# Kernel optimization log

Hardware: AMD Instinct MI355X
Metric: run time of the kernel (lower is better)

The kernel has to match this reference:

```python
import jax, jax.numpy as jnp
import numpy as np

SEGMENT_LENGTHS = [2048, 4096, 8192]
DILATION_RATES = [1, 2, 4]


def setup_inputs() -> dict:
    key = jax.random.key(0)
    kq, kk, kv = jax.random.split(key, 3)
    shape = (4, 8192, 16, 64)  # [b, seq, heads, head_dim]
    return {
        "query": jax.random.normal(kq, shape, dtype=jnp.float32),
        "key": jax.random.normal(kk, shape, dtype=jnp.float32),
        "value": jax.random.normal(kv, shape, dtype=jnp.float32),
    }


def _dilated_attention(query, key, value):
    b, S, h, d = query.shape
    num_groups = len(DILATION_RATES)
    # replicate torch group-size logic: h // ng each, first (h % ng) get +1
    group_sizes = [h // num_groups] * num_groups
    for i in range(h % num_groups):
        group_sizes[i] += 1

    scale = 1.0 / jnp.sqrt(jnp.asarray(d, dtype=query.dtype))
    out = jnp.zeros_like(query)

    for i, (g, r, s) in enumerate(zip(group_sizes, DILATION_RATES, SEGMENT_LENGTHS)):
        n = S // s
        offset = i % r
        hmin, hmax = i * g, (i + 1) * g  # faithful to original (uses current g)

        # gather strided segment views: [b, n, s', g, d]
        q = query.reshape(b, n, s, h, d)[:, :, offset::r, hmin:hmax, :]
        k = key.reshape(b, n, s, h, d)[:, :, offset::r, hmin:hmax, :]
        v = value.reshape(b, n, s, h, d)[:, :, offset::r, hmin:hmax, :]

        # NOTE: the original SDPA is applied to [., s', g, d], so attention
        # runs over the HEAD-group axis (length g) at each position.
        scores = jnp.einsum('bnsqd,bnskd->bnsqk', q, k) * scale
        attn = jax.nn.softmax(scores, axis=-1)
        x = jnp.einsum('bnsqk,bnskd->bnsqd', attn, v)  # [b, n, s', g, d]

        # normalize over (segment, position) dims, as in original
        x = x / x.sum(axis=(1, 2), keepdims=True)

        # scatter-add back into the output buffer
        out5 = out.reshape(b, n, s, h, d)
        out5 = out5.at[:, :, offset::r, hmin:hmax, :].add(x)
        out = out5.reshape(b, S, h, d)

    return out / num_groups


def reference(query, key, value):
    return _dilated_attention(query, key, value)
```

## Files before the change

### kernel.cpp

```cpp
#include <hip/hip_runtime.h>
#include <math.h>

#define BB 4
#define SS 8192
#define HH 16
#define DDIM 64

static const long X0_OFF = 6144;
static const long X0_SZ = 4L * 8192 * 6 * 64;
static const long X1_OFF = X0_OFF + X0_SZ;
static const long X1_SZ = 4L * 4096 * 5 * 64;
static const long X2_OFF = X1_OFF + X1_SZ;
static const long X2_SZ = 4L * 2048 * 5 * 64;
static const long WS_FLOATS = X2_OFF + X2_SZ;

__global__ __launch_bounds__(256) void k_zero_sums(float* ws) {
    int idx = blockIdx.x * 256 + threadIdx.x;
    if (idx < 6144) ws[idx] = 0.0f;
}

__device__ __forceinline__ float4 shfl_xor4(float4 v, int m) {
    return make_float4(__shfl_xor(v.x, m, 64), __shfl_xor(v.y, m, 64),
                       __shfl_xor(v.z, m, 64), __shfl_xor(v.w, m, 64));
}

__global__ __launch_bounds__(256) void k_attn(const float* __restrict__ Q,
                                              const float* __restrict__ Kp,
                                              const float* __restrict__ Vp,
                                              float* __restrict__ ws) {
    __shared__ __align__(16) float psum[4][6][64];

    int bid = blockIdx.x;
    int gi, b, tile, g, r, off, hmin, J;
    long xoff;
    if (bid < 2048)      { gi = 0; b = bid >> 9; tile = bid & 511; g = 6; r = 1; off = 0; hmin = 0;  J = 8192; xoff = X0_OFF; }
    else if (bid < 3072) { gi = 1; bid -= 2048; b = bid >> 8; tile = bid & 255; g = 5; r = 2; off = 1; hmin = 5;  J = 4096; xoff = X1_OFF; }
    else                 { gi = 2; bid -= 3072; b = bid >> 7; tile = bid & 127; g = 5; r = 4; off = 2; hmin = 10; J = 2048; xoff = X2_OFF; }

    const int t = threadIdx.x;
    const int lane = t & 63;
    const int wave = t >> 6;
    const int d4 = t & 15;
    const int pIdx = t >> 4;
    const int j = tile * 16 + pIdx;
    const int pos = off + j * r;

    const long rowbase = (((long)b * SS + pos) * HH + hmin) * DDIM;
    const float4* q4p = (const float4*)(Q + rowbase);
    const float4* k4p = (const float4*)(Kp + rowbase);
    const float4* v4p = (const float4*)(Vp + rowbase);

    float4 q4[6], k4[6], v4[6];
#pragma unroll
    for (int hh = 0; hh < 6; ++hh) {
        if (hh < g) {
            q4[hh] = q4p[hh * 16 + d4];
            k4[hh] = k4p[hh * 16 + d4];
            v4[hh] = v4p[hh * 16 + d4];
        } else {
            q4[hh] = make_float4(0.f, 0.f, 0.f, 0.f);
            k4[hh] = q4[hh];
            v4[hh] = q4[hh];
        }
    }

    float pp[6][6];
#pragma unroll
    for (int qh = 0; qh < 6; ++qh)
#pragma unroll
        for (int kh = 0; kh < 6; ++kh)
            pp[qh][kh] = q4[qh].x * k4[kh].x + q4[qh].y * k4[kh].y +
                         q4[qh].z * k4[kh].z + q4[qh].w * k4[kh].w;

#pragma unroll
    for (int m = 1; m <= 8; m <<= 1) {
#pragma unroll
        for (int qh = 0; qh < 6; ++qh)
#pragma unroll
            for (int kh = 0; kh < 6; ++kh)
                pp[qh][kh] += __shfl_xor(pp[qh][kh], m, 64);
    }

#pragma unroll
    for (int qh = 0; qh < 6; ++qh) {
        if (qh >= g) continue;
        float mx = pp[qh][0];
#pragma unroll
        for (int kh = 1; kh < 6; ++kh)
            if (kh < g) mx = fmaxf(mx, pp[qh][kh]);
        float den = 0.0f;
#pragma unroll
        for (int kh = 0; kh < 6; ++kh) {
            if (kh < g) { pp[qh][kh] = __expf((pp[qh][kh] - mx) * 0.125f); den += pp[qh][kh]; }
        }
        float rden = __frcp_rn(den);
#pragma unroll
        for (int kh = 0; kh < 6; ++kh) pp[qh][kh] *= rden;
    }

    float4* xrow = (float4*)(ws + xoff + (((long)b * J + j) * g) * DDIM);
    float4 o[6];
#pragma unroll
    for (int qh = 0; qh < 6; ++qh) {
        float4 acc = make_float4(0.f, 0.f, 0.f, 0.f);
        if (qh < g) {
#pragma unroll
            for (int kh = 0; kh < 6; ++kh) {
                if (kh < g) {
                    acc.x += pp[qh][kh] * v4[kh].x; acc.y += pp[qh][kh] * v4[kh].y;
                    acc.z += pp[qh][kh] * v4[kh].z; acc.w += pp[qh][kh] * v4[kh].w;
                }
            }
            xrow[qh * 16 + d4] = acc;
        }
        o[qh] = acc;
    }

#pragma unroll
    for (int m = 16; m <= 32; m <<= 1) {
#pragma unroll
        for (int qh = 0; qh < 6; ++qh) {
            float4 tmp = shfl_xor4(o[qh], m);
            o[qh].x += tmp.x; o[qh].y += tmp.y; o[qh].z += tmp.z; o[qh].w += tmp.w;
        }
    }
    if (lane < 16) {
#pragma unroll
        for (int qh = 0; qh < 6; ++qh)
            ((float4*)&psum[wave][qh][0])[d4] = o[qh];
    }
    __syncthreads();

    for (int idx = t; idx < g * 64; idx += 256) {
        int qh = idx >> 6, dd = idx & 63;
        float v = psum[0][qh][dd] + psum[1][qh][dd] + psum[2][qh][dd] + psum[3][qh][dd];
        unsafeAtomicAdd(ws + ((long)(gi * 4 + b) * 8 + qh) * 64 + dd, v);
    }
}

__global__ __launch_bounds__(256) void k_out(const float* __restrict__ ws,
                                             float* __restrict__ out) {
    const int t = threadIdx.x;
    const int bid = blockIdx.x;
    const int dd4 = t & 15;
    const int h = t >> 4;
    const int b = bid >> 10;
    const int pos0 = (bid & 1023) * 8;

    const bool has0 = (h < 6);
    const bool has1 = (h >= 5 && h <= 9);
    const bool has2 = (h >= 10 && h <= 14);

    float4 rs0 = make_float4(1.f, 1.f, 1.f, 1.f), rs1 = rs0, rs2 = rs0;
    if (has0) rs0 = ((const float4*)(ws + ((long)(0 * 4 + b) * 8 + h) * 64))[dd4];
    if (has1) rs1 = ((const float4*)(ws + ((long)(1 * 4 + b) * 8 + (h - 5)) * 64))[dd4];
    if (has2) rs2 = ((const float4*)(ws + ((long)(2 * 4 + b) * 8 + (h - 10)) * 64))[dd4];

    float4 x0[8], x1[4], x2[2];
    if (has0) {
#pragma unroll
        for (int pp = 0; pp < 8; ++pp)
            x0[pp] = ((const float4*)(ws + X0_OFF + (((long)b * 8192 + pos0 + pp) * 6 + h) * 64))[dd4];
    }
    if (has1) {
#pragma unroll
        for (int q = 0; q < 4; ++q) {
            int jj = (pos0 >> 1) + q;
            x1[q] = ((const float4*)(ws + X1_OFF + (((long)b * 4096 + jj) * 5 + (h - 5)) * 64))[dd4];
        }
    }
    if (has2) {
#pragma unroll
        for (int q = 0; q < 2; ++q) {
            int jj = (pos0 >> 2) + q;
            x2[q] = ((const float4*)(ws + X2_OFF + (((long)b * 2048 + jj) * 5 + (h - 10)) * 64))[dd4];
        }
    }

    if (has0) { rs0.x = __frcp_rn(rs0.x); rs0.y = __frcp_rn(rs0.y); rs0.z = __frcp_rn(rs0.z); rs0.w = __frcp_rn(rs0.w); }
    if (has1) { rs1.x = __frcp_rn(rs1.x); rs1.y = __frcp_rn(rs1.y); rs1.z = __frcp_rn(rs1.z); rs1.w = __frcp_rn(rs1.w); }
    if (has2) { rs2.x = __frcp_rn(rs2.x); rs2.y = __frcp_rn(rs2.y); rs2.z = __frcp_rn(rs2.z); rs2.w = __frcp_rn(rs2.w); }

    const float third = 1.0f / 3.0f;
#pragma unroll
    for (int pp = 0; pp < 8; ++pp) {
        float4 r = make_float4(0.f, 0.f, 0.f, 0.f);

        if (has0) {
            r.x += x0[pp].x * rs0.x; r.y += x0[pp].y * rs0.y;
            r.z += x0[pp].z * rs0.z; r.w += x0[pp].w * rs0.w;
        }
        if (has1 && (pp & 1) == 1) {
            int q = pp >> 1;
            r.x += x1[q].x * rs1.x; r.y += x1[q].y * rs1.y;
            r.z += x1[q].z * rs1.z; r.w += x1[q].w * rs1.w;
        }
        if (has2 && (pp & 3) == 2) {
            int q = pp >> 2;
            r.x += x2[q].x * rs2.x; r.y += x2[q].y * rs2.y;
            r.z += x2[q].z * rs2.z; r.w += x2[q].w * rs2.w;
        }

        r.x *= third; r.y *= third; r.z *= third; r.w *= third;
        ((float4*)out)[((long)(b * 8192 + pos0 + pp)) * 256 + t] = r;
    }
}

extern "C" void kernel_launch(void* const* d_in, const int* in_sizes, int n_in,
                              void* d_out, int out_size, void* d_ws, size_t ws_size,
                              hipStream_t stream) {
    const float* Q = (const float*)d_in[0];
    const float* K = (const float*)d_in[1];
    const float* V = (const float*)d_in[2];
    float* ws = (float*)d_ws;
    float* out = (float*)d_out;

    if (ws_size < (size_t)WS_FLOATS * sizeof(float)) return;

    k_zero_sums<<<24, 256, 0, stream>>>(ws);
    k_attn<<<3584, 256, 0, stream>>>(Q, K, V, ws);
    k_out<<<4096, 256, 0, stream>>>(ws, out);
}
```

Measured before the change: 396.7 us.

## Restructure attention via LDS-staged score tiles and deterministic partial-sum reduction

```diff
diff --git a/kernel.cpp b/kernel.cpp
--- a/kernel.cpp
+++ b/kernel.cpp
@@ -4,7 +4,6 @@
 #define BB 4
 #define SS 8192
 #define HH 16
-#define DDIM 64
 
 static const long X0_OFF = 6144;
 static const long X0_SZ = 4L * 8192 * 6 * 64;
@@ -12,130 +11,131 @@
 static const long X1_SZ = 4L * 4096 * 5 * 64;
 static const long X2_OFF = X1_OFF + X1_SZ;
 static const long X2_SZ = 4L * 2048 * 5 * 64;
-static const long WS_FLOATS = X2_OFF + X2_SZ;
+static const long PART_OFF = X2_OFF + X2_SZ;
+static const long SZP0 = 4L * 1024 * 384;
+static const long SZP1 = 4L * 512 * 384;
+static const long SZP2 = 4L * 256 * 384;
+static const long WS_SMALL = PART_OFF;
+static const long WS_FULL  = PART_OFF + SZP0 + SZP1 + SZP2;
 
 __global__ __launch_bounds__(256) void k_zero_sums(float* ws) {
     int idx = blockIdx.x * 256 + threadIdx.x;
     if (idx < 6144) ws[idx] = 0.0f;
 }
 
-__device__ __forceinline__ float4 shfl_xor4(float4 v, int m) {
-    return make_float4(__shfl_xor(v.x, m, 64), __shfl_xor(v.y, m, 64),
-                       __shfl_xor(v.z, m, 64), __shfl_xor(v.w, m, 64));
-}
-
-__global__ __launch_bounds__(256) void k_attn(const float* __restrict__ Q,
-                                              const float* __restrict__ Kp,
-                                              const float* __restrict__ Vp,
-                                              float* __restrict__ ws) {
-    __shared__ __align__(16) float psum[4][6][64];
-
-    int bid = blockIdx.x;
-    int gi, b, tile, g, r, off, hmin, J;
-    long xoff;
-    if (bid < 2048)      { gi = 0; b = bid >> 9; tile = bid & 511; g = 6; r = 1; off = 0; hmin = 0;  J = 8192; xoff = X0_OFF; }
-    else if (bid < 3072) { gi = 1; bid -= 2048; b = bid >> 8; tile = bid & 255; g = 5; r = 2; off = 1; hmin = 5;  J = 4096; xoff = X1_OFF; }
-    else                 { gi = 2; bid -= 3072; b = bid >> 7; tile = bid & 127; g = 5; r = 4; off = 2; hmin = 10; J = 2048; xoff = X2_OFF; }
+template<int G, int LTPB, int RR, int OFFS, int HMIN, int JJ, bool ATOMIC>
+__global__ __launch_bounds__(256) void k_attn2(const float* __restrict__ Q,
+                                               const float* __restrict__ K,
+                                               const float* __restrict__ V,
+                                               float* __restrict__ ws,
+                                               long xoff, long pbase, int gi) {
+    constexpr int P = 8;
+    constexpr int ROWS = P * G;
+    constexpr int STR = 17;
+    __shared__ __align__(16) float lq[ROWS * STR * 4];
+    __shared__ __align__(16) float lk[ROWS * STR * 4];
+    __shared__ float sc[P * G * G];
+    __shared__ float psum[384];
 
     const int t = threadIdx.x;
-    const int lane = t & 63;
-    const int wave = t >> 6;
-    const int d4 = t & 15;
-    const int pIdx = t >> 4;
-    const int j = tile * 16 + pIdx;
-    const int pos = off + j * r;
-
-    const long rowbase = (((long)b * SS + pos) * HH + hmin) * DDIM;
-    const float4* q4p = (const float4*)(Q + rowbase);
-    const float4* k4p = (const float4*)(Kp + rowbase);
-    const float4* v4p = (const float4*)(Vp + rowbase);
-
-    float4 q4[6], k4[6], v4[6];
-#pragma unroll
-    for (int hh = 0; hh < 6; ++hh) {
-        if (hh < g) {
-            q4[hh] = q4p[hh * 16 + d4];
-            k4[hh] = k4p[hh * 16 + d4];
-            v4[hh] = v4p[hh * 16 + d4];
-        } else {
-            q4[hh] = make_float4(0.f, 0.f, 0.f, 0.f);
-            k4[hh] = q4[hh];
-            v4[hh] = q4[hh];
-        }
-    }
-
-    float pp[6][6];
-#pragma unroll
-    for (int qh = 0; qh < 6; ++qh)
-#pragma unroll
-        for (int kh = 0; kh < 6; ++kh)
-            pp[qh][kh] = q4[qh].x * k4[kh].x + q4[qh].y * k4[kh].y +
-                         q4[qh].z * k4[kh].z + q4[qh].w * k4[kh].w;
-
-#pragma unroll
-    for (int m = 1; m <= 8; m <<= 1) {
-#pragma unroll
-        for (int qh = 0; qh < 6; ++qh)
-#pragma unroll
-            for (int kh = 0; kh < 6; ++kh)
-                pp[qh][kh] += __shfl_xor(pp[qh][kh], m, 64);
-    }
-
-#pragma unroll
-    for (int qh = 0; qh < 6; ++qh) {
-        if (qh >= g) continue;
-        float mx = pp[qh][0];
-#pragma unroll
-        for (int kh = 1; kh < 6; ++kh)
-            if (kh < g) mx = fmaxf(mx, pp[qh][kh]);
-        float den = 0.0f;
-#pragma unroll
-        for (int kh = 0; kh < 6; ++kh) {
-            if (kh < g) { pp[qh][kh] = __expf((pp[qh][kh] - mx) * 0.125f); den += pp[qh][kh]; }
-        }
-        float rden = __frcp_rn(den);
-#pragma unroll
-        for (int kh = 0; kh < 6; ++kh) pp[qh][kh] *= rden;
-    }
-
-    float4* xrow = (float4*)(ws + xoff + (((long)b * J + j) * g) * DDIM);
-    float4 o[6];
-#pragma unroll
-    for (int qh = 0; qh < 6; ++qh) {
+    const int bid = blockIdx.x;
+    const int b = bid >> LTPB;
+    const int tile = bid & ((1 << LTPB) - 1);
+    const int j0 = tile * P;
+
+    for (int i = t; i < 384; i += 256) psum[i] = 0.0f;
+
+    for (int e = t; e < ROWS * 16; e += 256) {
+        const int row = e >> 4, d4 = e & 15;
+        const int pos = row / G, hh = row - pos * G;
+        const long g16 = (((long)b * SS + OFFS + (long)(j0 + pos) * RR) * HH + HMIN + hh) * 16;
+        float4 qv = ((const float4*)Q)[g16 + d4];
+        float4 kv = ((const float4*)K)[g16 + d4];
+        *(float4*)&lq[(row * STR + d4) * 4] = qv;
+        *(float4*)&lk[(row * STR + d4) * 4] = kv;
+    }
+    __syncthreads();
+
+    for (int it = t; it < P * G * G; it += 256) {
+        const int pos = it / (G * G);
+        const int rem = it - pos * (G * G);
+        const int qh = rem / G, kh = rem - (rem / G) * G;
+        const float4* qr = (const float4*)&lq[(pos * G + qh) * STR * 4];
+        const float4* kr = (const float4*)&lk[(pos * G + kh) * STR * 4];
+        float4 a = make_float4(0.f, 0.f, 0.f, 0.f);
+#pragma unroll
+        for (int d4 = 0; d4 < 16; ++d4) {
+            float4 x = qr[d4], y = kr[d4];
+            a.x += x.x * y.x; a.y += x.y * y.y;
+            a.z += x.z * y.z; a.w += x.w * y.w;
+        }
+        sc[it] = (a.x + a.y) + (a.z + a.w);
+    }
+    __syncthreads();
+
+    if (t < P * G) {
+        float* row = &sc[t * G];
+        float mx = row[0];
+#pragma unroll
+        for (int k2 = 1; k2 < G; ++k2) mx = fmaxf(mx, row[k2]);
+        float e_[G];
+        float den = 0.f;
+#pragma unroll
+        for (int k2 = 0; k2 < G; ++k2) {
+            e_[k2] = __expf((row[k2] - mx) * 0.125f);
+            den += e_[k2];
+        }
+        const float rd = __frcp_rn(den);
+#pragma unroll
+        for (int k2 = 0; k2 < G; ++k2) row[k2] = e_[k2] * rd;
+    }
+    __syncthreads();
+
+    for (int it = t; it < P * G * 16; it += 256) {
+        const int pos = it / (G * 16);
+        const int rem = it - pos * (G * 16);
+        const int qh = rem >> 4, d4 = rem & 15;
+        const long vrow16 = (((long)b * SS + OFFS + (long)(j0 + pos) * RR) * HH + HMIN) * 16;
+        const float* pr = &sc[(pos * G + qh) * G];
         float4 acc = make_float4(0.f, 0.f, 0.f, 0.f);
-        if (qh < g) {
-#pragma unroll
-            for (int kh = 0; kh < 6; ++kh) {
-                if (kh < g) {
-                    acc.x += pp[qh][kh] * v4[kh].x; acc.y += pp[qh][kh] * v4[kh].y;
-                    acc.z += pp[qh][kh] * v4[kh].z; acc.w += pp[qh][kh] * v4[kh].w;
-                }
-            }
-            xrow[qh * 16 + d4] = acc;
-        }
-        o[qh] = acc;
-    }
-
-#pragma unroll
-    for (int m = 16; m <= 32; m <<= 1) {
-#pragma unroll
-        for (int qh = 0; qh < 6; ++qh) {
-            float4 tmp = shfl_xor4(o[qh], m);
-            o[qh].x += tmp.x; o[qh].y += tmp.y; o[qh].z += tmp.z; o[qh].w += tmp.w;
-        }
-    }
-    if (lane < 16) {
-#pragma unroll
-        for (int qh = 0; qh < 6; ++qh)
-            ((float4*)&psum[wave][qh][0])[d4] = o[qh];
-    }
-    __syncthreads();
-
-    for (int idx = t; idx < g * 64; idx += 256) {
-        int qh = idx >> 6, dd = idx & 63;
-        float v = psum[0][qh][dd] + psum[1][qh][dd] + psum[2][qh][dd] + psum[3][qh][dd];
-        unsafeAtomicAdd(ws + ((long)(gi * 4 + b) * 8 + qh) * 64 + dd, v);
-    }
+#pragma unroll
+        for (int kh = 0; kh < G; ++kh) {
+            float4 v4 = ((const float4*)V)[vrow16 + kh * 16 + d4];
+            const float pw = pr[kh];
+            acc.x += pw * v4.x; acc.y += pw * v4.y;
+            acc.z += pw * v4.z; acc.w += pw * v4.w;
+        }
+        ((float4*)(ws + xoff))[((long)(b * JJ + j0 + pos) * G + qh) * 16 + d4] = acc;
+        const int pb = (qh * 16 + d4) * 4;
+        atomicAdd(&psum[pb + 0], acc.x);
+        atomicAdd(&psum[pb + 1], acc.y);
+        atomicAdd(&psum[pb + 2], acc.z);
+        atomicAdd(&psum[pb + 3], acc.w);
+    }
+    __syncthreads();
+
+    if (ATOMIC) {
+        for (int i = t; i < G * 64; i += 256)
+            unsafeAtomicAdd(ws + (long)(gi * 4 + b) * 512 + i, psum[i]);
+    } else {
+        float* dst = ws + pbase + (long)bid * 384;
+        for (int i = t; i < 384; i += 256) dst[i] = psum[i];
+    }
+}
+
+__global__ __launch_bounds__(256) void k_sums(float* __restrict__ ws) {
+    const int o = blockIdx.x * 256 + threadIdx.x;
+    if (o >= 4608) return;
+    const int gi = o / 1536;
+    const int rem = o - gi * 1536;
+    const int b = rem / 384;
+    const int s = rem - b * 384;
+    const int nslots = 1024 >> gi;
+    const long gb = (gi == 0) ? 0 : ((gi == 1) ? SZP0 : (SZP0 + SZP1));
+    long base = PART_OFF + gb + ((long)b * nslots) * 384 + s;
+    float acc = 0.f;
+    for (int k2 = 0; k2 < nslots; ++k2) acc += ws[base + (long)k2 * 384];
+    ws[(long)(gi * 4 + b) * 512 + s] = acc;
 }
 
 __global__ __launch_bounds__(256) void k_out(const float* __restrict__ ws,
@@ -215,9 +215,19 @@
     float* ws = (float*)d_ws;
     float* out = (float*)d_out;
 
-    if (ws_size < (size_t)WS_FLOATS * sizeof(float)) return;
-
-    k_zero_sums<<<24, 256, 0, stream>>>(ws);
-    k_attn<<<3584, 256, 0, stream>>>(Q, K, V, ws);
+    const bool full = ws_size >= (size_t)WS_FULL * sizeof(float);
+    if (!full && ws_size < (size_t)WS_SMALL * sizeof(float)) return;
+
+    if (full) {
+        k_attn2<6, 10, 1, 0, 0,  8192, false><<<4096, 256, 0, stream>>>(Q, K, V, ws, X0_OFF, PART_OFF, 0);
+        k_attn2<5, 9,  2, 1, 5,  4096, false><<<2048, 256, 0, stream>>>(Q, K, V, ws, X1_OFF, PART_OFF + SZP0, 1);
+        k_attn2<5, 8,  4, 2, 10, 2048, false><<<1024, 256, 0, stream>>>(Q, K, V, ws, X2_OFF, PART_OFF + SZP0 + SZP1, 2);
+        k_sums<<<18, 256, 0, stream>>>(ws);
+    } else {
+        k_zero_sums<<<24, 256, 0, stream>>>(ws);
+        k_attn2<6, 10, 1, 0, 0,  8192, true><<<4096, 256, 0, stream>>>(Q, K, V, ws, X0_OFF, 0, 0);
+        k_attn2<5, 9,  2, 1, 5,  4096, true><<<2048, 256, 0, stream>>>(Q, K, V, ws, X1_OFF, 0, 1);
+        k_attn2<5, 8,  4, 2, 10, 2048, true><<<1024, 256, 0, stream>>>(Q, K, V, ws, X2_OFF, 0, 2);
+    }
     k_out<<<4096, 256, 0, stream>>>(ws, out);
 }
```

After: 777.9 us. +96.1%, slower.
